# Kernel optimization log

Measured on AMD Instinct MI355X. Metric: run time of the kernel, lower is better.

The kernel has to match this reference:

```python
import jax, jax.numpy as jnp
import numpy as np
from jax import lax

EMBED_DIM = 128
N_RELATIONS = 64
N_ENTITIES = 100000
N_EDGES = 600000


def setup_inputs() -> dict:
    key = jax.random.key(0)
    k1, k2, k3, k4, k5, k6 = jax.random.split(key, 6)
    entity_emb = jax.random.normal(k1, (N_ENTITIES, EMBED_DIM), dtype=jnp.float32)
    heads = jax.random.randint(k2, (N_EDGES,), 0, N_ENTITIES)
    rels = jax.random.randint(k3, (N_EDGES,), 0, N_RELATIONS)
    tails = jax.random.randint(k4, (N_EDGES,), 0, N_ENTITIES)
    # learned params: relation embedding table (std=0.01) and square Linear weight (xavier)
    rel_embed_weight = 0.01 * jax.random.normal(k5, (N_RELATIONS, EMBED_DIM), dtype=jnp.float32)
    xavier = float(np.sqrt(6.0 / (EMBED_DIM + EMBED_DIM)))
    W = jax.random.uniform(k6, (EMBED_DIM, EMBED_DIM), dtype=jnp.float32, minval=-xavier, maxval=xavier)
    return {"entity_emb": entity_emb, "rel_embed_weight": rel_embed_weight, "W": W,
            "heads": heads, "rels": rels, "tails": tails}


def reference(entity_emb, rel_embed_weight, W, heads, rels, tails):
    n_entities = entity_emb.shape[0]
    # gather edge endpoint / relation embeddings: [E, D]
    e_h = entity_emb[heads]
    e_t = entity_emb[tails]
    e_r = rel_embed_weight[rels]
    # tanh-gated dot-product score per edge: [E]
    score = jnp.sum(e_t * jnp.tanh(e_h + e_r), axis=-1)
    # global max-shift (detached in torch) then per-head segment softmax
    score_exp = jnp.exp(score - lax.stop_gradient(jnp.max(score)))
    score_sum = jax.ops.segment_sum(score_exp, heads, num_segments=n_entities)
    attn = score_exp / (score_sum[heads] + 1e-10)
    # scatter-add attention-weighted messages back to head nodes: [N, D]
    agg = jax.ops.segment_sum(attn[:, None] * e_t, heads, num_segments=n_entities)
    # final Linear (no bias) + LeakyReLU(0.2); dropout is identity in eval mode
    out = (entity_emb + agg) @ W.T
    return jax.nn.leaky_relu(out, negative_slope=0.2)
```

## Files before the change

### kernel.cpp

```cpp
#include <hip/hip_runtime.h>
#include <math.h>

#define EMBED 128
#define BMAX 8192
#define LDSPAD 136
#define DBINS 64

#define TWO_LOG2E 2.8853900817779268f

typedef __attribute__((ext_vector_type(8))) short short8;
typedef __attribute__((ext_vector_type(4))) float floatx4;

__device__ __forceinline__ float ex2(float x) { return __builtin_amdgcn_exp2f(x); }

__device__ __forceinline__ float fast_tanh2(float x) {
    float e = ex2(TWO_LOG2E * x);
    return 1.0f - 2.0f * __builtin_amdgcn_rcpf(1.0f + e);
}

__device__ __forceinline__ unsigned short f2b(float f) {
    union { float f; unsigned int u; } v; v.f = f;
    unsigned int r = v.u + 0x7FFFu + ((v.u >> 16) & 1u);
    return (unsigned short)(r >> 16);
}

__device__ __forceinline__ float b2f(short u) {
    union { float f; unsigned int i; } v;
    v.i = ((unsigned int)(unsigned short)u) << 16;
    return v.f;
}

__global__ __launch_bounds__(256) void k_cast_hist(
    const float* __restrict__ ent, const float* __restrict__ rel, const float* __restrict__ W,
    short* __restrict__ entb, short* __restrict__ relb, short* __restrict__ wb,
    const int* __restrict__ heads, int* __restrict__ cnt, int* __restrict__ ghist,
    int ngE, int ngR, int ngW, int E)
{
    if (blockIdx.x == 0 && threadIdx.x < DBINS) ghist[threadIdx.x] = 0;
    int stride = gridDim.x * 256;
    int total = ngE + ngR + ngW;
    for (int g = blockIdx.x * 256 + threadIdx.x; g < total; g += stride) {
        const float4* src; short* dst;
        if (g < ngE)            { src = (const float4*)ent + (size_t)g * 2;              dst = entb + (size_t)g * 8; }
        else if (g < ngE + ngR) { int g2 = g - ngE;       src = (const float4*)rel + (size_t)g2 * 2; dst = relb + (size_t)g2 * 8; }
        else                    { int g2 = g - ngE - ngR; src = (const float4*)W   + (size_t)g2 * 2; dst = wb   + (size_t)g2 * 8; }
        float4 a = src[0], b = src[1];
        short8 o;
        o[0] = (short)f2b(a.x); o[1] = (short)f2b(a.y); o[2] = (short)f2b(a.z); o[3] = (short)f2b(a.w);
        o[4] = (short)f2b(b.x); o[5] = (short)f2b(b.y); o[6] = (short)f2b(b.z); o[7] = (short)f2b(b.w);
        *(short8*)dst = o;
    }
    for (int e = blockIdx.x * 256 + threadIdx.x; e < E; e += stride)
        atomicAdd(cnt + heads[e], 1);
}

__global__ __launch_bounds__(1024) void k_scan1(
    const int* __restrict__ cnt, int* __restrict__ offs,
    int* __restrict__ bsum, int* __restrict__ ghist, int N)
{
    __shared__ int wsum[16];
    __shared__ int dh[DBINS];
    const int tid = threadIdx.x;
    if (tid < DBINS) dh[tid] = 0;
    int i = blockIdx.x * 1024 + tid;
    int v = (i < N) ? cnt[i] : 0;
    __syncthreads();
    if (i < N) atomicAdd(&dh[v < DBINS ? v : DBINS - 1], 1);
    int x = v;
    #pragma unroll
    for (int d = 1; d < 64; d <<= 1) {
        int y = __shfl_up(x, d, 64);
        if ((tid & 63) >= d) x += y;
    }
    if ((tid & 63) == 63) wsum[tid >> 6] = x;
    __syncthreads();
    if (tid < 16) {
        int w = wsum[tid];
        #pragma unroll
        for (int d = 1; d < 16; d <<= 1) {
            int y = __shfl_up(w, d, 16);
            if (tid >= d) w += y;
        }
        wsum[tid] = w;
    }
    __syncthreads();
    int add = (tid >= 64) ? wsum[(tid >> 6) - 1] : 0;
    int incl = x + add;
    if (i < N) offs[i] = incl - v;
    if (tid == 1023) bsum[blockIdx.x] = incl;
    if (tid < DBINS && dh[tid] > 0) atomicAdd(ghist + tid, dh[tid]);
}

__global__ __launch_bounds__(1024) void k_scan2(
    int* __restrict__ bsum, int* __restrict__ ghist, int* __restrict__ dbase, int nb)
{
    __shared__ int wsum[16];
    const int tid = threadIdx.x;
    int v = (tid < nb) ? bsum[tid] : 0;
    int x = v;
    #pragma unroll
    for (int d = 1; d < 64; d <<= 1) {
        int y = __shfl_up(x, d, 64);
        if ((tid & 63) >= d) x += y;
    }
    if ((tid & 63) == 63) wsum[tid >> 6] = x;
    __syncthreads();
    if (tid < 16) {
        int w = wsum[tid];
        #pragma unroll
        for (int d = 1; d < 16; d <<= 1) {
            int y = __shfl_up(w, d, 16);
            if (tid >= d) w += y;
        }
        wsum[tid] = w;
    }
    __syncthreads();
    int add = (tid >= 64) ? wsum[(tid >> 6) - 1] : 0;
    int incl = x + add;
    if (tid < nb) bsum[tid] = incl - v;
    if (tid < DBINS) {
        int g = ghist[tid];
        int s = g;
        #pragma unroll
        for (int d = 1; d < 64; d <<= 1) {
            int y = __shfl_up(s, d, 64);
            if (tid >= d) s += y;
        }
        dbase[tid] = s - g;
    }
}

__global__ __launch_bounds__(256) void k_scan3(
    int* __restrict__ offs, const int* __restrict__ bsum,
    int* __restrict__ cursor, const int* __restrict__ cnt,
    int* __restrict__ dbase, int* __restrict__ order, int N)
{
    __shared__ int lcnt[DBINS];
    __shared__ int lbase[DBINS];
    const int tid = threadIdx.x;
    if (tid < DBINS) lcnt[tid] = 0;
    __syncthreads();
    int i = blockIdx.x * 256 + tid;
    int deg = 0, lrank = 0;
    if (i < N) {
        int o = offs[i] + bsum[i >> 10];
        offs[i] = o;
        cursor[i] = o;
        int c = cnt[i];
        deg = c < DBINS ? c : DBINS - 1;
        lrank = atomicAdd(&lcnt[deg], 1);
    }
    __syncthreads();
    if (tid < DBINS) {
        int n = lcnt[tid];
        lbase[tid] = n > 0 ? atomicAdd(dbase + tid, n) : 0;
    }
    __syncthreads();
    if (i < N) order[lbase[deg] + lrank] = i;
}

__global__ __launch_bounds__(256) void k_csr(
    const int* __restrict__ heads, const int* __restrict__ rels,
    const int* __restrict__ tails, int* __restrict__ cursor,
    int2* __restrict__ tr, int E)
{
    int e = blockIdx.x * 256 + threadIdx.x;
    if (e >= E) return;
    int pos = atomicAdd(cursor + heads[e], 1);
    tr[pos] = make_int2(tails[e], rels[e]);
}

__global__ __launch_bounds__(256) void k_fused(
    const short* __restrict__ entb, const short* __restrict__ relb,
    const int* __restrict__ offs, const int* __restrict__ cnt,
    const int2* __restrict__ tr, const int* __restrict__ order,
    short* __restrict__ accb, float* __restrict__ mh, float* __restrict__ lh,
    float* __restrict__ blockmax, int N, int R)
{
    __shared__ short rl[64 * EMBED];
    const int tid = threadIdx.x;
    if (R <= 64) {
        int nch = R * 16;
        for (int i = tid; i < nch; i += 256)
            ((short8*)rl)[i] = ((const short8*)relb)[i];
    }
    __syncthreads();
    const short* relsrc = (R <= 64) ? (const short*)rl : relb;

    const int lane = tid & 15;
    int head0 = blockIdx.x * 16 + (tid >> 4);
    int head  = (head0 < N) ? order[head0] : N;
    float m = -INFINITY;
    if (head < N) {
        int start = offs[head];
        int c     = cnt[head];
        short8 hh = *((const short8*)(entb + (size_t)head * EMBED) + lane);
        float hf[8];
        #pragma unroll
        for (int i = 0; i < 8; ++i) hf[i] = b2f(hh[i]);
        float l = 0.f;
        float acc[8] = {0,0,0,0,0,0,0,0};
        for (int base = 0; base < c; base += 16) {
            int rem = c - base;
            int mm  = rem < 16 ? rem : 16;
            int2 trv = make_int2(0, 0);
            if (lane < mm) trv = tr[start + base + lane];
            for (int j = 0; j < mm; ++j) {
                int t = __shfl(trv.x, j, 16);
                int r = __shfl(trv.y, j, 16);
                short8 vt = *((const short8*)(entb + (size_t)t * EMBED) + lane);
                short8 vr = *((const short8*)(relsrc + (size_t)r * EMBED) + lane);
                float s = 0.f;
                #pragma unroll
                for (int i = 0; i < 8; ++i)
                    s += b2f(vt[i]) * fast_tanh2(hf[i] + b2f(vr[i]));
                s += __shfl_xor(s, 1, 16);
                s += __shfl_xor(s, 2, 16);
                s += __shfl_xor(s, 4, 16);
                s += __shfl_xor(s, 8, 16);
                float mn    = fmaxf(m, s);
                float alpha = __expf(m - mn);
                float p     = __expf(s - mn);
                l = l * alpha + p;
                #pragma unroll
                for (int q = 0; q < 8; ++q)
                    acc[q] = acc[q] * alpha + p * b2f(vt[q]);
                m = mn;
            }
        }
        short8 o;
        #pragma unroll
        for (int q = 0; q < 8; ++q) o[q] = (short)f2b(acc[q]);
        *((short8*)(accb + (size_t)head * EMBED) + lane) = o;
        if (lane == 0) { mh[head] = m; lh[head] = l; }
    }
    __shared__ float smax[256];
    smax[tid] = m;
    __syncthreads();
    for (int off = 128; off > 0; off >>= 1) {
        if (tid < off) smax[tid] = fmaxf(smax[tid], smax[tid + off]);
        __syncthreads();
    }
    if (tid == 0) blockmax[blockIdx.x] = smax[0];
}

__global__ __launch_bounds__(256) void k_maxred(
    const float* __restrict__ blockmax, float* __restrict__ Mout, int n)
{
    __shared__ float smax[256];
    float m = -INFINITY;
    for (int i = threadIdx.x; i < n; i += 256) m = fmaxf(m, blockmax[i]);
    smax[threadIdx.x] = m;
    __syncthreads();
    for (int off = 128; off > 0; off >>= 1) {
        if ((int)threadIdx.x < off)
            smax[threadIdx.x] = fmaxf(smax[threadIdx.x], smax[threadIdx.x + off]);
        __syncthreads();
    }
    if (threadIdx.x == 0) Mout[0] = smax[0];
}

__global__ __launch_bounds__(256) void k_gemm_f(
    const short* __restrict__ entb, const short* __restrict__ accb,
    const float* __restrict__ mh, const float* __restrict__ lh,
    const float* __restrict__ Mptr, const short* __restrict__ wb,
    float* __restrict__ out, int N)
{
    __shared__ short xs[128 * LDSPAD];
    __shared__ short ws[128 * LDSPAD];
    const int tid = threadIdx.x;
    const int n0  = blockIdx.x * 128;
    const float M = Mptr[0];

    #pragma unroll
    for (int it = 0; it < 8; ++it) {
        int ch = it * 256 + tid;
        int row = ch >> 4, col8 = ch & 15;
        *(short8*)(ws + row * LDSPAD + col8 * 8) = ((const short8*)wb)[ch];
    }
    #pragma unroll
    for (int it = 0; it < 8; ++it) {
        int ch = it * 256 + tid;
        int row = ch >> 4, col8 = ch & 15;
        int g = n0 + row;
        short8 v = {0,0,0,0,0,0,0,0};
        if (g < N) {
            float inv = 1.0f / (lh[g] + 1e-10f * __expf(M - mh[g]));
            short8 e8 = *((const short8*)(entb + (size_t)g * EMBED) + col8);
            short8 a8 = *((const short8*)(accb + (size_t)g * EMBED) + col8);
            #pragma unroll
            for (int q = 0; q < 8; ++q)
                v[q] = (short)f2b(b2f(e8[q]) + b2f(a8[q]) * inv);
        }
        *(short8*)(xs + row * LDSPAD + col8 * 8) = v;
    }
    __syncthreads();

    const int wv   = tid >> 6;
    const int lane = tid & 63;
    const int n16  = lane & 15;
    const int quad = lane >> 4;

    floatx4 acc[2][8];
    #pragma unroll
    for (int rt = 0; rt < 2; ++rt)
        #pragma unroll
        for (int jt = 0; jt < 8; ++jt)
            acc[rt][jt] = (floatx4){0.f, 0.f, 0.f, 0.f};

    #pragma unroll
    for (int kc = 0; kc < 4; ++kc) {
        int koff = kc * 32 + quad * 8;
        short8 a0 = *(const short8*)(xs + (wv * 32      + n16) * LDSPAD + koff);
        short8 a1 = *(const short8*)(xs + (wv * 32 + 16 + n16) * LDSPAD + koff);
        #pragma unroll
        for (int jt = 0; jt < 8; ++jt) {
            short8 b = *(const short8*)(ws + (jt * 16 + n16) * LDSPAD + koff);
            acc[0][jt] = __builtin_amdgcn_mfma_f32_16x16x32_bf16(a0, b, acc[0][jt], 0, 0, 0);
            acc[1][jt] = __builtin_amdgcn_mfma_f32_16x16x32_bf16(a1, b, acc[1][jt], 0, 0, 0);
        }
    }

    #pragma unroll
    for (int rt = 0; rt < 2; ++rt) {
        int rowbase = n0 + wv * 32 + rt * 16 + quad * 4;
        #pragma unroll
        for (int r = 0; r < 4; ++r) {
            int grow = rowbase + r;
            if (grow < N) {
                float* o = out + (size_t)grow * EMBED + n16;
                #pragma unroll
                for (int jt = 0; jt < 8; ++jt) {
                    float v = acc[rt][jt][r];
                    o[jt * 16] = (v > 0.f) ? v : 0.2f * v;
                }
            }
        }
    }
}

extern "C" void kernel_launch(void* const* d_in, const int* in_sizes, int n_in,
                              void* d_out, int out_size, void* d_ws, size_t ws_size,
                              hipStream_t stream)
{
    const float* ent   = (const float*)d_in[0];
    const float* rel   = (const float*)d_in[1];
    const float* W     = (const float*)d_in[2];
    const int*   heads = (const int*)d_in[3];
    const int*   rels  = (const int*)d_in[4];
    const int*   tails = (const int*)d_in[5];
    const int E = in_sizes[3];
    const int N = in_sizes[0] / EMBED;
    const int R = in_sizes[1] / EMBED;
    float* out = (float*)d_out;

    short* accb     = (short*)d_ws;
    float* mh       = (float*)(accb + (size_t)N * EMBED);
    float* lh       = mh + N;
    int2*  tr       = (int2*)(lh + N);
    int*   cnt      = (int*)(tr + E);
    int*   offs     = cnt + N;
    int*   cursor   = offs + N;
    float* blockmax = (float*)(cursor + N);
    float* Mval     = blockmax + BMAX;
    int*   bsum     = (int*)(Mval + 4);
    int*   ghist    = bsum + 1024;
    int*   dbase    = ghist + DBINS;
    int*   order    = dbase + DBINS;
    short* wb       = (short*)(order + N);
    short* entb     = wb + 16384;
    short* relb     = entb + (size_t)N * EMBED;

    const int nb  = (N + 1023) >> 10;
    const int ngh = (N + 15) / 16;

    hipMemsetAsync(cnt, 0, (size_t)N * sizeof(int), stream);

    int ngE = N * EMBED / 8, ngR = R * EMBED / 8, ngW = EMBED * EMBED / 8;
    k_cast_hist<<<2048, 256, 0, stream>>>(ent, rel, W, entb, relb, wb, heads, cnt, ghist, ngE, ngR, ngW, E);
    k_scan1<<<nb, 1024, 0, stream>>>(cnt, offs, bsum, ghist, N);
    k_scan2<<<1, 1024, 0, stream>>>(bsum, ghist, dbase, nb);
    k_scan3<<<(N + 255) / 256, 256, 0, stream>>>(offs, bsum, cursor, cnt, dbase, order, N);
    k_csr<<<(E + 255) / 256, 256, 0, stream>>>(heads, rels, tails, cursor, tr, E);
    k_fused<<<ngh, 256, 0, stream>>>(entb, relb, offs, cnt, tr, order, accb, mh, lh, blockmax, N, R);
    k_maxred<<<1, 256, 0, stream>>>(blockmax, Mval, ngh);
    k_gemm_f<<<(N + 127) / 128, 256, 0, stream>>>(entb, accb, mh, lh, Mval, wb, out, N);
}
```

Baseline: 250.8 us.

## Fuse scan kernels, defer softmax rescale, use DPP reductions in edge loop

```diff
diff --git a/kernel.cpp b/kernel.cpp
--- a/kernel.cpp
+++ b/kernel.cpp
@@ -7,6 +7,7 @@
 #define DBINS 64
 
 #define TWO_LOG2E 2.8853900817779268f
+#define DEFER_THR 32.0f
 
 typedef __attribute__((ext_vector_type(8))) short short8;
 typedef __attribute__((ext_vector_type(4))) float floatx4;
@@ -28,6 +29,19 @@
     union { float f; unsigned int i; } v;
     v.i = ((unsigned int)(unsigned short)u) << 16;
     return v.f;
+}
+
+template <int CTRL>
+__device__ __forceinline__ float dpp_add_f(float x) {
+    int y = __builtin_amdgcn_update_dpp(0, __float_as_int(x), CTRL, 0xF, 0xF, false);
+    return x + __int_as_float(y);
+}
+__device__ __forceinline__ float dpp_sum16(float s) {
+    s = dpp_add_f<0x121>(s);
+    s = dpp_add_f<0x122>(s);
+    s = dpp_add_f<0x124>(s);
+    s = dpp_add_f<0x128>(s);
+    return s;
 }
 
 __global__ __launch_bounds__(256) void k_cast_hist(
@@ -91,11 +105,19 @@
     if (tid < DBINS && dh[tid] > 0) atomicAdd(ghist + tid, dh[tid]);
 }
 
-__global__ __launch_bounds__(1024) void k_scan2(
-    int* __restrict__ bsum, int* __restrict__ ghist, int* __restrict__ dbase, int nb)
-{
-    __shared__ int wsum[16];
+__global__ __launch_bounds__(256) void k_scan23(
+    int* __restrict__ offs, const int* __restrict__ bsum,
+    int* __restrict__ cursor, const int* __restrict__ cnt,
+    const int* __restrict__ ghist, int* __restrict__ bincur,
+    int* __restrict__ order, int N, int nb)
+{
+    __shared__ int sb[256];
+    __shared__ int ws4[4];
+    __shared__ int dbs[DBINS];
+    __shared__ int lcnt[DBINS];
+    __shared__ int lbase[DBINS];
     const int tid = threadIdx.x;
+
     int v = (tid < nb) ? bsum[tid] : 0;
     int x = v;
     #pragma unroll
@@ -103,22 +125,22 @@
         int y = __shfl_up(x, d, 64);
         if ((tid & 63) >= d) x += y;
     }
-    if ((tid & 63) == 63) wsum[tid >> 6] = x;
-    __syncthreads();
-    if (tid < 16) {
-        int w = wsum[tid];
-        #pragma unroll
-        for (int d = 1; d < 16; d <<= 1) {
-            int y = __shfl_up(w, d, 16);
+    if ((tid & 63) == 63) ws4[tid >> 6] = x;
+    __syncthreads();
+    if (tid < 4) {
+        int w = ws4[tid];
+        #pragma unroll
+        for (int d = 1; d < 4; d <<= 1) {
+            int y = __shfl_up(w, d, 4);
             if (tid >= d) w += y;
         }
-        wsum[tid] = w;
-    }
-    __syncthreads();
-    int add = (tid >= 64) ? wsum[(tid >> 6) - 1] : 0;
-    int incl = x + add;
-    if (tid < nb) bsum[tid] = incl - v;
-    if (tid < DBINS) {
+        ws4[tid] = w;
+    }
+    __syncthreads();
+    int add = (tid >= 64) ? ws4[(tid >> 6) - 1] : 0;
+    sb[tid] = x + add - v;
+
+    if (tid < 64) {
         int g = ghist[tid];
         int s = g;
         #pragma unroll
@@ -126,24 +148,15 @@
             int y = __shfl_up(s, d, 64);
             if (tid >= d) s += y;
         }
-        dbase[tid] = s - g;
-    }
-}
-
-__global__ __launch_bounds__(256) void k_scan3(
-    int* __restrict__ offs, const int* __restrict__ bsum,
-    int* __restrict__ cursor, const int* __restrict__ cnt,
-    int* __restrict__ dbase, int* __restrict__ order, int N)
-{
-    __shared__ int lcnt[DBINS];
-    __shared__ int lbase[DBINS];
-    const int tid = threadIdx.x;
+        dbs[tid] = s - g;
+    }
     if (tid < DBINS) lcnt[tid] = 0;
     __syncthreads();
+
     int i = blockIdx.x * 256 + tid;
     int deg = 0, lrank = 0;
     if (i < N) {
-        int o = offs[i] + bsum[i >> 10];
+        int o = offs[i] + sb[i >> 10];
         offs[i] = o;
         cursor[i] = o;
         int c = cnt[i];
@@ -153,7 +166,7 @@
     __syncthreads();
     if (tid < DBINS) {
         int n = lcnt[tid];
-        lbase[tid] = n > 0 ? atomicAdd(dbase + tid, n) : 0;
+        lbase[tid] = (n > 0) ? (dbs[tid] + atomicAdd(bincur + tid, n)) : 0;
     }
     __syncthreads();
     if (i < N) order[lbase[deg] + lrank] = i;
@@ -190,7 +203,7 @@
     const int lane = tid & 15;
     int head0 = blockIdx.x * 16 + (tid >> 4);
     int head  = (head0 < N) ? order[head0] : N;
-    float m = -INFINITY;
+    float mt = -INFINITY;
     if (head < N) {
         int start = offs[head];
         int c     = cnt[head];
@@ -198,6 +211,7 @@
         float hf[8];
         #pragma unroll
         for (int i = 0; i < 8; ++i) hf[i] = b2f(hh[i]);
+        float m = -INFINITY;
         float l = 0.f;
         float acc[8] = {0,0,0,0,0,0,0,0};
         for (int base = 0; base < c; base += 16) {
@@ -211,21 +225,28 @@
                 short8 vt = *((const short8*)(entb + (size_t)t * EMBED) + lane);
                 short8 vr = *((const short8*)(relsrc + (size_t)r * EMBED) + lane);
                 float s = 0.f;
+                float vtf[8];
                 #pragma unroll
-                for (int i = 0; i < 8; ++i)
-                    s += b2f(vt[i]) * fast_tanh2(hf[i] + b2f(vr[i]));
-                s += __shfl_xor(s, 1, 16);
-                s += __shfl_xor(s, 2, 16);
-                s += __shfl_xor(s, 4, 16);
-                s += __shfl_xor(s, 8, 16);
-                float mn    = fmaxf(m, s);
-                float alpha = __expf(m - mn);
-                float p     = __expf(s - mn);
-                l = l * alpha + p;
+                for (int i = 0; i < 8; ++i) {
+                    vtf[i] = b2f(vt[i]);
+                    s = fmaf(vtf[i], fast_tanh2(hf[i] + b2f(vr[i])), s);
+                }
+                s = dpp_sum16(s);
+                mt = fmaxf(mt, s);
+                float dlt = s - m;
+                if (dlt > DEFER_THR) {
+                    float alpha = __expf(-dlt);
+                    l *= alpha;
+                    #pragma unroll
+                    for (int q = 0; q < 8; ++q) acc[q] *= alpha;
+                    m = s;
+                    dlt = 0.f;
+                }
+                float p = __expf(dlt);
+                l += p;
                 #pragma unroll
                 for (int q = 0; q < 8; ++q)
-                    acc[q] = acc[q] * alpha + p * b2f(vt[q]);
-                m = mn;
+                    acc[q] = fmaf(p, vtf[q], acc[q]);
             }
         }
         short8 o;
@@ -235,7 +256,7 @@
         if (lane == 0) { mh[head] = m; lh[head] = l; }
     }
     __shared__ float smax[256];
-    smax[tid] = m;
+    smax[tid] = mt;
     __syncthreads();
     for (int off = 128; off > 0; off >>= 1) {
         if (tid < off) smax[tid] = fmaxf(smax[tid], smax[tid + off]);
@@ -268,16 +289,22 @@
 {
     __shared__ short xs[128 * LDSPAD];
     __shared__ short ws[128 * LDSPAD];
+    __shared__ float invs[128];
     const int tid = threadIdx.x;
     const int n0  = blockIdx.x * 128;
     const float M = Mptr[0];
 
+    if (tid < 128) {
+        int g = n0 + tid;
+        invs[tid] = (g < N) ? 1.0f / (lh[g] + 1e-10f * __expf(M - mh[g])) : 0.f;
+    }
     #pragma unroll
     for (int it = 0; it < 8; ++it) {
         int ch = it * 256 + tid;
         int row = ch >> 4, col8 = ch & 15;
         *(short8*)(ws + row * LDSPAD + col8 * 8) = ((const short8*)wb)[ch];
     }
+    __syncthreads();
     #pragma unroll
     for (int it = 0; it < 8; ++it) {
         int ch = it * 256 + tid;
@@ -285,7 +312,7 @@
         int g = n0 + row;
         short8 v = {0,0,0,0,0,0,0,0};
         if (g < N) {
-            float inv = 1.0f / (lh[g] + 1e-10f * __expf(M - mh[g]));
+            float inv = invs[row];
             short8 e8 = *((const short8*)(entb + (size_t)g * EMBED) + col8);
             short8 a8 = *((const short8*)(accb + (size_t)g * EMBED) + col8);
             #pragma unroll
@@ -359,14 +386,14 @@
     float* lh       = mh + N;
     int2*  tr       = (int2*)(lh + N);
     int*   cnt      = (int*)(tr + E);
-    int*   offs     = cnt + N;
+    int*   bincur   = cnt + N;
+    int*   offs     = bincur + DBINS;
     int*   cursor   = offs + N;
     float* blockmax = (float*)(cursor + N);
     float* Mval     = blockmax + BMAX;
     int*   bsum     = (int*)(Mval + 4);
     int*   ghist    = bsum + 1024;
-    int*   dbase    = ghist + DBINS;
-    int*   order    = dbase + DBINS;
+    int*   order    = ghist + DBINS;
     short* wb       = (short*)(order + N);
     short* entb     = wb + 16384;
     short* relb     = entb + (size_t)N * EMBED;
@@ -374,13 +401,12 @@
     const int nb  = (N + 1023) >> 10;
     const int ngh = (N + 15) / 16;
 
-    hipMemsetAsync(cnt, 0, (size_t)N * sizeof(int), stream);
+    hipMemsetAsync(cnt, 0, (size_t)(N + DBINS) * sizeof(int), stream);
 
     int ngE = N * EMBED / 8, ngR = R * EMBED / 8, ngW = EMBED * EMBED / 8;
     k_cast_hist<<<2048, 256, 0, stream>>>(ent, rel, W, entb, relb, wb, heads, cnt, ghist, ngE, ngR, ngW, E);
     k_scan1<<<nb, 1024, 0, stream>>>(cnt, offs, bsum, ghist, N);
-    k_scan2<<<1, 1024, 0, stream>>>(bsum, ghist, dbase, nb);
-    k_scan3<<<(N + 255) / 256, 256, 0, stream>>>(offs, bsum, cursor, cnt, dbase, order, N);
+    k_scan23<<<(N + 255) / 256, 256, 0, stream>>>(offs, bsum, cursor, cnt, ghist, bincur, order, N, nb);
     k_csr<<<(E + 255) / 256, 256, 0, stream>>>(heads, rels, tails, cursor, tr, E);
     k_fused<<<ngh, 256, 0, stream>>>(entb, relb, offs, cnt, tr, order, accb, mh, lh, blockmax, N, R);
     k_maxred<<<1, 256, 0, stream>>>(blockmax, Mval, ngh);
```

Result: faster. 242.5 us (-3.3%).
